# Performance work log

Measured on AMD Instinct MI355X. Metric: run time of the kernel, lower is better.

## Reference

```python
import jax, jax.numpy as jnp
import numpy as np

N_NODES = 100000


def _sage_conv(x, edge_index, w_l, w_r, b):
    # PyG SAGEConv (mean aggr, root_weight=True):
    #   out_i = W_l @ mean_{j in N(i)} x_j + b + W_r @ x_i
    # edge_index[0] = source nodes, edge_index[1] = destination nodes.
    src, dst = edge_index[0], edge_index[1]
    msgs = x[src]  # [E, C_in]
    summed = jax.ops.segment_sum(msgs, dst, num_segments=N_NODES)  # [N, C_in]
    deg = jax.ops.segment_sum(jnp.ones((src.shape[0],), x.dtype), dst,
                              num_segments=N_NODES)
    mean = summed / jnp.maximum(deg, 1.0)[:, None]
    return mean @ w_l.T + b + x @ w_r.T


def setup_inputs() -> dict:
    key = jax.random.key(0)
    ks = jax.random.split(key, 12)
    C_IN, C_H, C_OUT = 32, 64, 1
    E = 1600000

    def glorot(k, shape):
        fan_in = shape[1]
        return jax.random.uniform(k, shape, jnp.float32,
                                  -1.0 / np.sqrt(fan_in), 1.0 / np.sqrt(fan_in))

    x = jax.random.normal(ks[0], (N_NODES, C_IN), jnp.float32)
    edge_index = jax.random.randint(ks[1], (2, E), 0, N_NODES, jnp.int64)
    return {
        "x": x,
        "edge_index": edge_index,
        "w_l1": glorot(ks[2], (C_H, C_IN)),
        "w_r1": glorot(ks[3], (C_H, C_IN)),
        "b1": jnp.zeros((C_H,), jnp.float32),
        "w_l2": glorot(ks[4], (C_H, C_H)),
        "w_r2": glorot(ks[5], (C_H, C_H)),
        "b2": jnp.zeros((C_H,), jnp.float32),
        "w_l3": glorot(ks[6], (C_OUT, C_H)),
        "w_r3": glorot(ks[7], (C_OUT, C_H)),
        "b3": jnp.zeros((C_OUT,), jnp.float32),
    }


def reference(x, edge_index, w_l1, w_r1, b1, w_l2, w_r2, b2, w_l3, w_r3, b3):
    h = jax.nn.relu(_sage_conv(x, edge_index, w_l1, w_r1, b1))
    h = jax.nn.relu(_sage_conv(h, edge_index, w_l2, w_r2, b2))
    h = _sage_conv(h, edge_index, w_l3, w_r3, b3)
    return jax.nn.sigmoid(h)
```

## Files before the change

kernel.cpp:

```cpp
#include <hip/hip_runtime.h>
#include <math.h>

#define NN 100000
#define CAP 48
#define ZROW NN
#define XCONV_NB 3125

#define PART_NB 1024
#define STRIDE4 (PART_NB * 256 * 4)
#define BUKN 256
#define NBUK 391
#define NREP 8
#define LCAPR 768

typedef float  v4f __attribute__((ext_vector_type(4)));
typedef int    v4i __attribute__((ext_vector_type(4)));
typedef float  v2f __attribute__((ext_vector_type(2)));

__device__ __forceinline__ unsigned short f2bf(float v) {
    unsigned int u = __float_as_uint(v);
    u += 0x7FFFu + ((u >> 16) & 1u);
    return (unsigned short)(u >> 16);
}
__device__ __forceinline__ float bf2f(unsigned short b) {
    return __uint_as_float(((unsigned int)b) << 16);
}
__device__ __forceinline__ float bflo(unsigned int u) {
    return __uint_as_float(u << 16);
}
__device__ __forceinline__ float bfhi(unsigned int u) {
    return __uint_as_float(u & 0xFFFF0000u);
}
__device__ __forceinline__ unsigned int pack2bf(float a, float b) {
    return (unsigned)f2bf(a) | ((unsigned)f2bf(b) << 16);
}

__global__ __launch_bounds__(256) void part_kernel(
    const int* __restrict__ ei, int* __restrict__ gcur, unsigned int* __restrict__ lists,
    int E, const float* __restrict__ x, unsigned char* __restrict__ xf8,
    unsigned char* __restrict__ h1f8, int xtotal) {
    if (blockIdx.x >= PART_NB) {
        int t = threadIdx.x;
        if (blockIdx.x == PART_NB) {
            if (t < 16) ((unsigned int*)(h1f8 + (size_t)NN * 64))[t] = 0;
            else if (t < 24) ((unsigned int*)(xf8 + (size_t)NN * 32))[t - 16] = 0;
        }
        int i = ((blockIdx.x - PART_NB) * 256 + t) * 4;
        if (i + 3 < xtotal) {
            float4 v = *(const float4*)(x + i);
            int w = __builtin_amdgcn_cvt_pk_fp8_f32(v.x, v.y, 0, false);
            w = __builtin_amdgcn_cvt_pk_fp8_f32(v.z, v.w, w, true);
            *(unsigned int*)(xf8 + i) = (unsigned int)w;
        } else if (i < xtotal) {
            for (int j = i; j < xtotal; ++j) {
                int w = __builtin_amdgcn_cvt_pk_fp8_f32(x[j], 0.f, 0, false);
                xf8[j] = (unsigned char)(w & 0xFF);
            }
        }
        return;
    }
    __shared__ int lcnt[NBUK], lbase[NBUK];
    int t = threadIdx.x;
    for (int i = t; i < NBUK; i += 256) lcnt[i] = 0;
    __syncthreads();

    const int* dsts = ei + E;
    unsigned int ent[8];
    int eb[8], rk[8];
    bool val[8];
    int base0 = (blockIdx.x * 256 + t) * 4;
    int rep = blockIdx.x & (NREP - 1);

#pragma unroll
    for (int it = 0; it < 2; ++it) {
        int e0 = base0 + it * STRIDE4;
        if (e0 + 3 < E) {
            v4i d = *(const v4i*)(dsts + e0);
            v4i s = *(const v4i*)(ei + e0);
            int dd[4] = {d.x, d.y, d.z, d.w};
            int ss[4] = {s.x, s.y, s.z, s.w};
#pragma unroll
            for (int j = 0; j < 4; ++j) {
                int k = it * 4 + j;
                int b = dd[j] >> 8;
                eb[k] = b;
                ent[k] = ((unsigned int)(dd[j] & 255) << 17) | (unsigned int)ss[j];
                val[k] = true;
                rk[k] = atomicAdd(&lcnt[b], 1);
            }
        } else {
#pragma unroll
            for (int j = 0; j < 4; ++j) {
                int k = it * 4 + j;
                int e = e0 + j;
                val[k] = (e < E);
                eb[k] = 0; ent[k] = 0; rk[k] = 0;
                if (e < E) {
                    int dv = dsts[e];
                    int b = dv >> 8;
                    eb[k] = b;
                    ent[k] = ((unsigned int)(dv & 255) << 17) | (unsigned int)ei[e];
                    rk[k] = atomicAdd(&lcnt[b], 1);
                }
            }
        }
    }
    __syncthreads();
    for (int i = t; i < NBUK; i += 256)
        lbase[i] = atomicAdd(&gcur[rep * NBUK + i], lcnt[i]);
    __syncthreads();
#pragma unroll
    for (int k = 0; k < 8; ++k) {
        if (val[k]) {
            int pos = lbase[eb[k]] + rk[k];
            if (pos < LCAPR)
                lists[((size_t)eb[k] * NREP + rep) * LCAPR + pos] = ent[k];
        }
    }
}

__global__ __launch_bounds__(256) void fill_kernel(
    const unsigned int* __restrict__ lists, const int* __restrict__ gcur,
    int* __restrict__ cnt, int* __restrict__ csr) {
    __shared__ int lc[BUKN];
    __shared__ int tile[BUKN * CAP];
    int b = blockIdx.x, t = threadIdx.x;
    lc[t] = 0;
    for (int i = t; i < BUKN * CAP; i += 256) tile[i] = ZROW;
    __syncthreads();
    for (int rep = 0; rep < NREP; ++rep) {
        int total = gcur[rep * NBUK + b];
        if (total > LCAPR) total = LCAPR;
        const unsigned int* lg = lists + ((size_t)b * NREP + rep) * LCAPR;
        for (int e = t; e < total; e += 256) {
            unsigned int ent = lg[e];
            int dl = (int)(ent >> 17);
            int pos = atomicAdd(&lc[dl], 1);
            if (pos < CAP) tile[dl * CAP + pos] = (int)(ent & 0x1FFFFu);
        }
    }
    __syncthreads();
    int nodes = NN - b * BUKN;
    if (nodes > BUKN) nodes = BUKN;
    if (t < nodes) cnt[b * BUKN + t] = lc[t];
    int tot = nodes * CAP;
    int gbase = b * BUKN * CAP;
    for (int i = t * 4; i < tot; i += 1024)
        *(v4i*)(csr + gbase + i) = *(const v4i*)(tile + i);
}


__global__ __launch_bounds__(256) void agg1_kernel(
    const unsigned char* __restrict__ xf8, const int* __restrict__ cnt,
    const int* __restrict__ csr, unsigned int* __restrict__ mean1b, int n) {
    int t = threadIdx.x;
    int lane = t & 63, wv = t >> 6;
    int p = lane & 7, q = lane >> 3;
    int ngrp = (n + 3) >> 2;
    for (int grp = blockIdx.x; grp < ngrp; grp += gridDim.x) {
        int node = __builtin_amdgcn_readfirstlane(grp * 4 + wv);
        if (node >= n) continue;
        int deg = cnt[node];
        int len = (deg < CAP) ? deg : CAP;
        int lenp = (len + 31) & ~31;
        int base = node * CAP;
        float aA[4] = {0.f, 0.f, 0.f, 0.f}, aB[4] = {0.f, 0.f, 0.f, 0.f};
        float aC[4] = {0.f, 0.f, 0.f, 0.f}, aD[4] = {0.f, 0.f, 0.f, 0.f};
        for (int i = 0; i < lenp; i += 32) {
            int i0 = __builtin_nontemporal_load(csr + base + i + q);
            int i1 = __builtin_nontemporal_load(csr + base + i + 8 + q);
            int i2 = __builtin_nontemporal_load(csr + base + i + 16 + q);
            int i3 = __builtin_nontemporal_load(csr + base + i + 24 + q);
            unsigned int u0 = *(const unsigned int*)(xf8 + (size_t)i0 * 32 + 4 * p);
            unsigned int u1 = *(const unsigned int*)(xf8 + (size_t)i1 * 32 + 4 * p);
            unsigned int u2 = *(const unsigned int*)(xf8 + (size_t)i2 * 32 + 4 * p);
            unsigned int u3 = *(const unsigned int*)(xf8 + (size_t)i3 * 32 + 4 * p);
            v2f l0 = __builtin_amdgcn_cvt_pk_f32_fp8((int)u0, false);
            v2f h0 = __builtin_amdgcn_cvt_pk_f32_fp8((int)u0, true);
            v2f l1 = __builtin_amdgcn_cvt_pk_f32_fp8((int)u1, false);
            v2f h1 = __builtin_amdgcn_cvt_pk_f32_fp8((int)u1, true);
            v2f l2 = __builtin_amdgcn_cvt_pk_f32_fp8((int)u2, false);
            v2f h2 = __builtin_amdgcn_cvt_pk_f32_fp8((int)u2, true);
            v2f l3 = __builtin_amdgcn_cvt_pk_f32_fp8((int)u3, false);
            v2f h3 = __builtin_amdgcn_cvt_pk_f32_fp8((int)u3, true);
            aA[0] += l0.x; aA[1] += l0.y; aA[2] += h0.x; aA[3] += h0.y;
            aB[0] += l1.x; aB[1] += l1.y; aB[2] += h1.x; aB[3] += h1.y;
            aC[0] += l2.x; aC[1] += l2.y; aC[2] += h2.x; aC[3] += h2.y;
            aD[0] += l3.x; aD[1] += l3.y; aD[2] += h3.x; aD[3] += h3.y;
        }
        float s[4];
#pragma unroll
        for (int k = 0; k < 4; ++k) {
            float v = (aA[k] + aB[k]) + (aC[k] + aD[k]);
            v += __shfl_xor(v, 8, 64);
            v += __shfl_xor(v, 16, 64);
            v += __shfl_xor(v, 32, 64);
            s[k] = v;
        }
        float inv = 1.0f / (float)(deg > 1 ? deg : 1);
        if (q == 0) {
            uint2 o;
            o.x = pack2bf(s[0] * inv, s[1] * inv);
            o.y = pack2bf(s[2] * inv, s[3] * inv);
            *(uint2*)(mean1b + (size_t)node * 16 + p * 2) = o;
        }
    }
}

__global__ __launch_bounds__(256) void agg2_kernel(
    const unsigned char* __restrict__ h1f8, const int* __restrict__ cnt,
    const int* __restrict__ csr, unsigned int* __restrict__ mean2b, int n) {
    int t = threadIdx.x;
    int lane = t & 63, wv = t >> 6;
    int p = lane & 15, q = lane >> 4;
    int ngrp = (n + 3) >> 2;
    for (int grp = blockIdx.x; grp < ngrp; grp += gridDim.x) {
        int node = __builtin_amdgcn_readfirstlane(grp * 4 + wv);
        if (node >= n) continue;
        int deg = cnt[node];
        int len = (deg < CAP) ? deg : CAP;
        int lenp = (len + 15) & ~15;
        int base = node * CAP;
        float aA[4] = {0.f, 0.f, 0.f, 0.f}, aB[4] = {0.f, 0.f, 0.f, 0.f};
        float aC[4] = {0.f, 0.f, 0.f, 0.f}, aD[4] = {0.f, 0.f, 0.f, 0.f};
        for (int i = 0; i < lenp; i += 16) {
            int i0 = __builtin_nontemporal_load(csr + base + i + q);
            int i1 = __builtin_nontemporal_load(csr + base + i + 4 + q);
            int i2 = __builtin_nontemporal_load(csr + base + i + 8 + q);
            int i3 = __builtin_nontemporal_load(csr + base + i + 12 + q);
            unsigned int u0 = *(const unsigned int*)(h1f8 + (size_t)i0 * 64 + 4 * p);
            unsigned int u1 = *(const unsigned int*)(h1f8 + (size_t)i1 * 64 + 4 * p);
            unsigned int u2 = *(const unsigned int*)(h1f8 + (size_t)i2 * 64 + 4 * p);
            unsigned int u3 = *(const unsigned int*)(h1f8 + (size_t)i3 * 64 + 4 * p);
            v2f l0 = __builtin_amdgcn_cvt_pk_f32_fp8((int)u0, false);
            v2f h0 = __builtin_amdgcn_cvt_pk_f32_fp8((int)u0, true);
            v2f l1 = __builtin_amdgcn_cvt_pk_f32_fp8((int)u1, false);
            v2f h1 = __builtin_amdgcn_cvt_pk_f32_fp8((int)u1, true);
            v2f l2 = __builtin_amdgcn_cvt_pk_f32_fp8((int)u2, false);
            v2f h2 = __builtin_amdgcn_cvt_pk_f32_fp8((int)u2, true);
            v2f l3 = __builtin_amdgcn_cvt_pk_f32_fp8((int)u3, false);
            v2f h3 = __builtin_amdgcn_cvt_pk_f32_fp8((int)u3, true);
            aA[0] += l0.x; aA[1] += l0.y; aA[2] += h0.x; aA[3] += h0.y;
            aB[0] += l1.x; aB[1] += l1.y; aB[2] += h1.x; aB[3] += h1.y;
            aC[0] += l2.x; aC[1] += l2.y; aC[2] += h2.x; aC[3] += h2.y;
            aD[0] += l3.x; aD[1] += l3.y; aD[2] += h3.x; aD[3] += h3.y;
        }
        float s[4];
#pragma unroll
        for (int k = 0; k < 4; ++k) {
            float v = (aA[k] + aB[k]) + (aC[k] + aD[k]);
            v += __shfl_xor(v, 16, 64);
            v += __shfl_xor(v, 32, 64);
            s[k] = v;
        }
        float inv = 1.0f / (float)(deg > 1 ? deg : 1);
        if (q == 0) {
            uint2 o;
            o.x = pack2bf(s[0] * inv, s[1] * inv);
            o.y = pack2bf(s[2] * inv, s[3] * inv);
            *(uint2*)(mean2b + (size_t)node * 32 + p * 2) = o;
        }
    }
}

template<int HALF, bool FINAL, bool A1BF>
__global__ __launch_bounds__(256) void lin_kernel(
    const unsigned short* __restrict__ a0b,
    const float* __restrict__ a1f, const unsigned short* __restrict__ a1b,
    const float* __restrict__ w0, const float* __restrict__ w1,
    const float* __restrict__ bias,
    const float* __restrict__ wl3, const float* __restrict__ wr3,
    unsigned short* __restrict__ outb, unsigned char* __restrict__ outf8,
    float* __restrict__ z, float* __restrict__ r, int n) {
    const int KC = 32;
    const int K = 2 * HALF;
    __shared__ float A_s[KC * 132];
    __shared__ float B_s[KC * 68];
    int t = threadIdx.x;
    int tx = t & 7;
    int ty = t >> 3;
    int oc0 = tx * 8;
    int node0 = ty * 4;
    int nb = blockIdx.x * 128;
    float acc[4][8];
#pragma unroll
    for (int i = 0; i < 4; ++i)
#pragma unroll
        for (int j = 0; j < 8; ++j) acc[i][j] = 0.f;

    for (int c = 0; c < K / KC; ++c) {
        int koff = c * KC;
        bool useA1 = (koff >= HALF);
        const float* wsrc = useA1 ? w1 : w0;
        int klo = koff % HALF;
        __syncthreads();
        for (int i = t * 4; i < 128 * KC; i += 1024) {
            int nd = i >> 5, kk = i & 31;
            int gnode = nb + nd;
            float v0 = 0.f, v1 = 0.f, v2 = 0.f, v3 = 0.f;
            if (gnode < n) {
                if (!useA1) {
                    uint2 u = *(const uint2*)(a0b + (size_t)gnode * HALF + klo + kk);
                    v0 = bflo(u.x); v1 = bfhi(u.x); v2 = bflo(u.y); v3 = bfhi(u.y);
                } else if (A1BF) {
                    uint2 u = *(const uint2*)(a1b + (size_t)gnode * HALF + klo + kk);
                    v0 = bflo(u.x); v1 = bfhi(u.x); v2 = bflo(u.y); v3 = bfhi(u.y);
                } else {
                    float4 f = *(const float4*)(a1f + (size_t)gnode * HALF + klo + kk);
                    v0 = f.x; v1 = f.y; v2 = f.z; v3 = f.w;
                }
            }
            A_s[kk * 132 + nd] = v0;
            A_s[(kk + 1) * 132 + nd] = v1;
            A_s[(kk + 2) * 132 + nd] = v2;
            A_s[(kk + 3) * 132 + nd] = v3;
        }
        for (int i = t * 4; i < 64 * KC; i += 1024) {
            int oc = i >> 5, kk = i & 31;
            float4 f = *(const float4*)(wsrc + oc * HALF + klo + kk);
            B_s[kk * 68 + oc] = f.x;
            B_s[(kk + 1) * 68 + oc] = f.y;
            B_s[(kk + 2) * 68 + oc] = f.z;
            B_s[(kk + 3) * 68 + oc] = f.w;
        }
        __syncthreads();
#pragma unroll 8
        for (int kk = 0; kk < KC; ++kk) {
            float4 av = *(const float4*)&A_s[kk * 132 + node0];
            float4 b0 = *(const float4*)&B_s[kk * 68 + oc0];
            float4 b1v = *(const float4*)&B_s[kk * 68 + oc0 + 4];
            float aa[4] = {av.x, av.y, av.z, av.w};
            float bb[8] = {b0.x, b0.y, b0.z, b0.w, b1v.x, b1v.y, b1v.z, b1v.w};
#pragma unroll
            for (int i = 0; i < 4; ++i)
#pragma unroll
                for (int j = 0; j < 8; ++j) acc[i][j] += aa[i] * bb[j];
        }
    }

    float bv[8];
#pragma unroll
    for (int j = 0; j < 8; ++j) bv[j] = bias[oc0 + j];

    if (!FINAL) {
#pragma unroll
        for (int i = 0; i < 4; ++i) {
            int node = nb + node0 + i;
            if (node < n) {
                float o[8];
#pragma unroll
                for (int j = 0; j < 8; ++j) o[j] = fmaxf(acc[i][j] + bv[j], 0.f);
                uint4 pk;
                pk.x = pack2bf(o[0], o[1]);
                pk.y = pack2bf(o[2], o[3]);
                pk.z = pack2bf(o[4], o[5]);
                pk.w = pack2bf(o[6], o[7]);
                *(uint4*)&outb[(size_t)node * 64 + oc0] = pk;
                int w0i = __builtin_amdgcn_cvt_pk_fp8_f32(o[0], o[1], 0, false);
                w0i = __builtin_amdgcn_cvt_pk_fp8_f32(o[2], o[3], w0i, true);
                int w1i = __builtin_amdgcn_cvt_pk_fp8_f32(o[4], o[5], 0, false);
                w1i = __builtin_amdgcn_cvt_pk_fp8_f32(o[6], o[7], w1i, true);
                uint2 pk8;
                pk8.x = (unsigned int)w0i;
                pk8.y = (unsigned int)w1i;
                *(uint2*)(outf8 + (size_t)node * 64 + oc0) = pk8;
            }
        }
    } else {
        float w3l[8], w3r[8];
#pragma unroll
        for (int j = 0; j < 8; ++j) { w3l[j] = wl3[oc0 + j]; w3r[j] = wr3[oc0 + j]; }
#pragma unroll
        for (int i = 0; i < 4; ++i) {
            float zz = 0.f, rr = 0.f;
#pragma unroll
            for (int j = 0; j < 8; ++j) {
                float h2 = fmaxf(acc[i][j] + bv[j], 0.f);
                zz += h2 * w3l[j];
                rr += h2 * w3r[j];
            }
#pragma unroll
            for (int o = 1; o < 8; o <<= 1) {
                zz += __shfl_xor(zz, o, 64);
                rr += __shfl_xor(rr, o, 64);
            }
            int node = nb + node0 + i;
            if (tx == 0 && node < n) { z[node] = zz; r[node] = rr; }
        }
    }
}

__global__ void final_kernel(const float* __restrict__ z, const float* __restrict__ r,
                             const int* __restrict__ cnt, const int* __restrict__ csr,
                             const float* __restrict__ b3, float* __restrict__ out, int n) {
    int t = threadIdx.x;
    int lane = t & 63, wv = t >> 6;
    int node = __builtin_amdgcn_readfirstlane(blockIdx.x * 4 + wv);
    if (node >= n) return;
    int deg = cnt[node];
    int len = (deg < CAP) ? deg : CAP;
    float acc = 0.f;
    if (lane < len) acc = z[csr[node * CAP + lane]];
#pragma unroll
    for (int o = 32; o > 0; o >>= 1) acc += __shfl_down(acc, o, 64);
    if (lane == 0) {
        float m = acc / (float)(deg > 1 ? deg : 1);
        out[node] = 1.0f / (1.0f + expf(-(m + r[node] + b3[0])));
    }
}

extern "C" void kernel_launch(void* const* d_in, const int* in_sizes, int n_in,
                              void* d_out, int out_size, void* d_ws, size_t ws_size,
                              hipStream_t stream) {
    const float* x   = (const float*)d_in[0];
    const int*   ei  = (const int*)d_in[1];
    const float* wl1 = (const float*)d_in[2];
    const float* wr1 = (const float*)d_in[3];
    const float* b1  = (const float*)d_in[4];
    const float* wl2 = (const float*)d_in[5];
    const float* wr2 = (const float*)d_in[6];
    const float* b2  = (const float*)d_in[7];
    const float* wl3 = (const float*)d_in[8];
    const float* wr3 = (const float*)d_in[9];
    const float* b3  = (const float*)d_in[10];
    float* out = (float*)d_out;

    const int E = in_sizes[1] / 2;
    const int n = NN;

    int* cnt = (int*)d_ws;
    int* gcur = cnt + n;
    int* csr = gcur + NREP * NBUK + 8;
    float* z = (float*)(csr + (size_t)n * CAP);
    float* r = z + n;
    unsigned char*  xf8 = (unsigned char*)(r + n);
    unsigned short* h1b = (unsigned short*)(xf8 + (size_t)(n + 1) * 32);
    unsigned char*  h1f8 = (unsigned char*)(h1b + (size_t)(n + 1) * 64);
    unsigned short* mb  = (unsigned short*)(h1f8 + (size_t)(n + 1) * 64);
    unsigned int* lists = (unsigned int*)mb;

    hipMemsetAsync(gcur, 0, sizeof(int) * (NREP * NBUK + 8), stream);
    part_kernel<<<PART_NB + XCONV_NB, 256, 0, stream>>>(ei, gcur, lists, E, x, xf8, h1f8, n * 32);
    fill_kernel<<<NBUK, 256, 0, stream>>>(lists, gcur, cnt, csr);

    int gemm_grid = (n + 127) / 128;

    agg1_kernel<<<2048, 256, 0, stream>>>(xf8, cnt, csr, (unsigned int*)mb, n);
    lin_kernel<32, false, false><<<gemm_grid, 256, 0, stream>>>(
        mb, x, nullptr, wl1, wr1, b1, nullptr, nullptr, h1b, h1f8, nullptr, nullptr, n);

    agg2_kernel<<<2048, 256, 0, stream>>>(h1f8, cnt, csr, (unsigned int*)mb, n);
    lin_kernel<64, true, true><<<gemm_grid, 256, 0, stream>>>(
        mb, nullptr, h1b, wl2, wr2, b2, wl3, wr3, nullptr, nullptr, z, r, n);

    final_kernel<<<(n + 3) / 4, 256, 0, stream>>>(z, r, cnt, csr, b3, out, n);
}
```

Measured before the change: 251.9 us.

## Fuse neighbor mean aggregation into the linear GEMM kernels via shared memory

Merges the separate aggregation kernels into the SAGE linear kernels. Each 128-node block now computes its own neighbor means from the fp8 features and stores them as bf16 in shared memory instead of writing them to global memory and reading them back. This removes a global round trip of the mean tensor and two kernel launches. The cost is extra shared memory and a long serial aggregation phase per block before the GEMM, which may lower occupancy and latency hiding compared with the 2048-block grid-stride aggregation.

```diff
diff --git a/kernel.cpp b/kernel.cpp
--- a/kernel.cpp
+++ b/kernel.cpp
@@ -149,124 +149,11 @@
         *(v4i*)(csr + gbase + i) = *(const v4i*)(tile + i);
 }
 
-
-__global__ __launch_bounds__(256) void agg1_kernel(
-    const unsigned char* __restrict__ xf8, const int* __restrict__ cnt,
-    const int* __restrict__ csr, unsigned int* __restrict__ mean1b, int n) {
-    int t = threadIdx.x;
-    int lane = t & 63, wv = t >> 6;
-    int p = lane & 7, q = lane >> 3;
-    int ngrp = (n + 3) >> 2;
-    for (int grp = blockIdx.x; grp < ngrp; grp += gridDim.x) {
-        int node = __builtin_amdgcn_readfirstlane(grp * 4 + wv);
-        if (node >= n) continue;
-        int deg = cnt[node];
-        int len = (deg < CAP) ? deg : CAP;
-        int lenp = (len + 31) & ~31;
-        int base = node * CAP;
-        float aA[4] = {0.f, 0.f, 0.f, 0.f}, aB[4] = {0.f, 0.f, 0.f, 0.f};
-        float aC[4] = {0.f, 0.f, 0.f, 0.f}, aD[4] = {0.f, 0.f, 0.f, 0.f};
-        for (int i = 0; i < lenp; i += 32) {
-            int i0 = __builtin_nontemporal_load(csr + base + i + q);
-            int i1 = __builtin_nontemporal_load(csr + base + i + 8 + q);
-            int i2 = __builtin_nontemporal_load(csr + base + i + 16 + q);
-            int i3 = __builtin_nontemporal_load(csr + base + i + 24 + q);
-            unsigned int u0 = *(const unsigned int*)(xf8 + (size_t)i0 * 32 + 4 * p);
-            unsigned int u1 = *(const unsigned int*)(xf8 + (size_t)i1 * 32 + 4 * p);
-            unsigned int u2 = *(const unsigned int*)(xf8 + (size_t)i2 * 32 + 4 * p);
-            unsigned int u3 = *(const unsigned int*)(xf8 + (size_t)i3 * 32 + 4 * p);
-            v2f l0 = __builtin_amdgcn_cvt_pk_f32_fp8((int)u0, false);
-            v2f h0 = __builtin_amdgcn_cvt_pk_f32_fp8((int)u0, true);
-            v2f l1 = __builtin_amdgcn_cvt_pk_f32_fp8((int)u1, false);
-            v2f h1 = __builtin_amdgcn_cvt_pk_f32_fp8((int)u1, true);
-            v2f l2 = __builtin_amdgcn_cvt_pk_f32_fp8((int)u2, false);
-            v2f h2 = __builtin_amdgcn_cvt_pk_f32_fp8((int)u2, true);
-            v2f l3 = __builtin_amdgcn_cvt_pk_f32_fp8((int)u3, false);
-            v2f h3 = __builtin_amdgcn_cvt_pk_f32_fp8((int)u3, true);
-            aA[0] += l0.x; aA[1] += l0.y; aA[2] += h0.x; aA[3] += h0.y;
-            aB[0] += l1.x; aB[1] += l1.y; aB[2] += h1.x; aB[3] += h1.y;
-            aC[0] += l2.x; aC[1] += l2.y; aC[2] += h2.x; aC[3] += h2.y;
-            aD[0] += l3.x; aD[1] += l3.y; aD[2] += h3.x; aD[3] += h3.y;
-        }
-        float s[4];
-#pragma unroll
-        for (int k = 0; k < 4; ++k) {
-            float v = (aA[k] + aB[k]) + (aC[k] + aD[k]);
-            v += __shfl_xor(v, 8, 64);
-            v += __shfl_xor(v, 16, 64);
-            v += __shfl_xor(v, 32, 64);
-            s[k] = v;
-        }
-        float inv = 1.0f / (float)(deg > 1 ? deg : 1);
-        if (q == 0) {
-            uint2 o;
-            o.x = pack2bf(s[0] * inv, s[1] * inv);
-            o.y = pack2bf(s[2] * inv, s[3] * inv);
-            *(uint2*)(mean1b + (size_t)node * 16 + p * 2) = o;
-        }
-    }
-}
-
-__global__ __launch_bounds__(256) void agg2_kernel(
-    const unsigned char* __restrict__ h1f8, const int* __restrict__ cnt,
-    const int* __restrict__ csr, unsigned int* __restrict__ mean2b, int n) {
-    int t = threadIdx.x;
-    int lane = t & 63, wv = t >> 6;
-    int p = lane & 15, q = lane >> 4;
-    int ngrp = (n + 3) >> 2;
-    for (int grp = blockIdx.x; grp < ngrp; grp += gridDim.x) {
-        int node = __builtin_amdgcn_readfirstlane(grp * 4 + wv);
-        if (node >= n) continue;
-        int deg = cnt[node];
-        int len = (deg < CAP) ? deg : CAP;
-        int lenp = (len + 15) & ~15;
-        int base = node * CAP;
-        float aA[4] = {0.f, 0.f, 0.f, 0.f}, aB[4] = {0.f, 0.f, 0.f, 0.f};
-        float aC[4] = {0.f, 0.f, 0.f, 0.f}, aD[4] = {0.f, 0.f, 0.f, 0.f};
-        for (int i = 0; i < lenp; i += 16) {
-            int i0 = __builtin_nontemporal_load(csr + base + i + q);
-            int i1 = __builtin_nontemporal_load(csr + base + i + 4 + q);
-            int i2 = __builtin_nontemporal_load(csr + base + i + 8 + q);
-            int i3 = __builtin_nontemporal_load(csr + base + i + 12 + q);
-            unsigned int u0 = *(const unsigned int*)(h1f8 + (size_t)i0 * 64 + 4 * p);
-            unsigned int u1 = *(const unsigned int*)(h1f8 + (size_t)i1 * 64 + 4 * p);
-            unsigned int u2 = *(const unsigned int*)(h1f8 + (size_t)i2 * 64 + 4 * p);
-            unsigned int u3 = *(const unsigned int*)(h1f8 + (size_t)i3 * 64 + 4 * p);
-            v2f l0 = __builtin_amdgcn_cvt_pk_f32_fp8((int)u0, false);
-            v2f h0 = __builtin_amdgcn_cvt_pk_f32_fp8((int)u0, true);
-            v2f l1 = __builtin_amdgcn_cvt_pk_f32_fp8((int)u1, false);
-            v2f h1 = __builtin_amdgcn_cvt_pk_f32_fp8((int)u1, true);
-            v2f l2 = __builtin_amdgcn_cvt_pk_f32_fp8((int)u2, false);
-            v2f h2 = __builtin_amdgcn_cvt_pk_f32_fp8((int)u2, true);
-            v2f l3 = __builtin_amdgcn_cvt_pk_f32_fp8((int)u3, false);
-            v2f h3 = __builtin_amdgcn_cvt_pk_f32_fp8((int)u3, true);
-            aA[0] += l0.x; aA[1] += l0.y; aA[2] += h0.x; aA[3] += h0.y;
-            aB[0] += l1.x; aB[1] += l1.y; aB[2] += h1.x; aB[3] += h1.y;
-            aC[0] += l2.x; aC[1] += l2.y; aC[2] += h2.x; aC[3] += h2.y;
-            aD[0] += l3.x; aD[1] += l3.y; aD[2] += h3.x; aD[3] += h3.y;
-        }
-        float s[4];
-#pragma unroll
-        for (int k = 0; k < 4; ++k) {
-            float v = (aA[k] + aB[k]) + (aC[k] + aD[k]);
-            v += __shfl_xor(v, 16, 64);
-            v += __shfl_xor(v, 32, 64);
-            s[k] = v;
-        }
-        float inv = 1.0f / (float)(deg > 1 ? deg : 1);
-        if (q == 0) {
-            uint2 o;
-            o.x = pack2bf(s[0] * inv, s[1] * inv);
-            o.y = pack2bf(s[2] * inv, s[3] * inv);
-            *(uint2*)(mean2b + (size_t)node * 32 + p * 2) = o;
-        }
-    }
-}
-
-template<int HALF, bool FINAL, bool A1BF>
-__global__ __launch_bounds__(256) void lin_kernel(
-    const unsigned short* __restrict__ a0b,
-    const float* __restrict__ a1f, const unsigned short* __restrict__ a1b,
+template<int HALF, bool FINAL>
+__global__ __launch_bounds__(256) void flin_kernel(
+    const unsigned char* __restrict__ gf8,
+    const float* __restrict__ selff, const unsigned short* __restrict__ selfb,
+    const int* __restrict__ cnt, const int* __restrict__ csr,
     const float* __restrict__ w0, const float* __restrict__ w1,
     const float* __restrict__ bias,
     const float* __restrict__ wl3, const float* __restrict__ wr3,
@@ -274,14 +161,115 @@
     float* __restrict__ z, float* __restrict__ r, int n) {
     const int KC = 32;
     const int K = 2 * HALF;
+    __shared__ unsigned int M_su[(HALF / 2) * 132];
     __shared__ float A_s[KC * 132];
     __shared__ float B_s[KC * 68];
     int t = threadIdx.x;
+    int lane = t & 63, wv = t >> 6;
+    int nb = blockIdx.x * 128;
+
+    if (HALF == 32) {
+        int p = lane & 7, q = lane >> 3;
+        for (int g = 0; g < 32; ++g) {
+            int rnd = g * 4 + wv;
+            int node = nb + rnd;
+            int deg = (node < n) ? cnt[node] : 0;
+            int len = (deg < CAP) ? deg : CAP;
+            int lenp = (len + 31) & ~31;
+            int base = node * CAP;
+            float aA[4] = {0.f, 0.f, 0.f, 0.f}, aB[4] = {0.f, 0.f, 0.f, 0.f};
+            float aC[4] = {0.f, 0.f, 0.f, 0.f}, aD[4] = {0.f, 0.f, 0.f, 0.f};
+            for (int i = 0; i < lenp; i += 32) {
+                int i0 = __builtin_nontemporal_load(csr + base + i + q);
+                int i1 = __builtin_nontemporal_load(csr + base + i + 8 + q);
+                int i2 = __builtin_nontemporal_load(csr + base + i + 16 + q);
+                int i3 = __builtin_nontemporal_load(csr + base + i + 24 + q);
+                unsigned int u0 = *(const unsigned int*)(gf8 + (size_t)i0 * 32 + 4 * p);
+                unsigned int u1 = *(const unsigned int*)(gf8 + (size_t)i1 * 32 + 4 * p);
+                unsigned int u2 = *(const unsigned int*)(gf8 + (size_t)i2 * 32 + 4 * p);
+                unsigned int u3 = *(const unsigned int*)(gf8 + (size_t)i3 * 32 + 4 * p);
+                v2f l0 = __builtin_amdgcn_cvt_pk_f32_fp8((int)u0, false);
+                v2f h0 = __builtin_amdgcn_cvt_pk_f32_fp8((int)u0, true);
+                v2f l1 = __builtin_amdgcn_cvt_pk_f32_fp8((int)u1, false);
+                v2f h1 = __builtin_amdgcn_cvt_pk_f32_fp8((int)u1, true);
+                v2f l2 = __builtin_amdgcn_cvt_pk_f32_fp8((int)u2, false);
+                v2f h2 = __builtin_amdgcn_cvt_pk_f32_fp8((int)u2, true);
+                v2f l3 = __builtin_amdgcn_cvt_pk_f32_fp8((int)u3, false);
+                v2f h3 = __builtin_amdgcn_cvt_pk_f32_fp8((int)u3, true);
+                aA[0] += l0.x; aA[1] += l0.y; aA[2] += h0.x; aA[3] += h0.y;
+                aB[0] += l1.x; aB[1] += l1.y; aB[2] += h1.x; aB[3] += h1.y;
+                aC[0] += l2.x; aC[1] += l2.y; aC[2] += h2.x; aC[3] += h2.y;
+                aD[0] += l3.x; aD[1] += l3.y; aD[2] += h3.x; aD[3] += h3.y;
+            }
+            float s[4];
+#pragma unroll
+            for (int k = 0; k < 4; ++k) {
+                float v = (aA[k] + aB[k]) + (aC[k] + aD[k]);
+                v += __shfl_xor(v, 8, 64);
+                v += __shfl_xor(v, 16, 64);
+                v += __shfl_xor(v, 32, 64);
+                s[k] = v;
+            }
+            float inv = 1.0f / (float)(deg > 1 ? deg : 1);
+            if (q == 0) {
+                M_su[(2 * p) * 132 + rnd] = pack2bf(s[0] * inv, s[1] * inv);
+                M_su[(2 * p + 1) * 132 + rnd] = pack2bf(s[2] * inv, s[3] * inv);
+            }
+        }
+    } else {
+        int p = lane & 15, q = lane >> 4;
+        for (int g = 0; g < 32; ++g) {
+            int rnd = g * 4 + wv;
+            int node = nb + rnd;
+            int deg = (node < n) ? cnt[node] : 0;
+            int len = (deg < CAP) ? deg : CAP;
+            int lenp = (len + 15) & ~15;
+            int base = node * CAP;
+            float aA[4] = {0.f, 0.f, 0.f, 0.f}, aB[4] = {0.f, 0.f, 0.f, 0.f};
+            float aC[4] = {0.f, 0.f, 0.f, 0.f}, aD[4] = {0.f, 0.f, 0.f, 0.f};
+            for (int i = 0; i < lenp; i += 16) {
+                int i0 = __builtin_nontemporal_load(csr + base + i + q);
+                int i1 = __builtin_nontemporal_load(csr + base + i + 4 + q);
+                int i2 = __builtin_nontemporal_load(csr + base + i + 8 + q);
+                int i3 = __builtin_nontemporal_load(csr + base + i + 12 + q);
+                unsigned int u0 = *(const unsigned int*)(gf8 + (size_t)i0 * 64 + 4 * p);
+                unsigned int u1 = *(const unsigned int*)(gf8 + (size_t)i1 * 64 + 4 * p);
+                unsigned int u2 = *(const unsigned int*)(gf8 + (size_t)i2 * 64 + 4 * p);
+                unsigned int u3 = *(const unsigned int*)(gf8 + (size_t)i3 * 64 + 4 * p);
+                v2f l0 = __builtin_amdgcn_cvt_pk_f32_fp8((int)u0, false);
+                v2f h0 = __builtin_amdgcn_cvt_pk_f32_fp8((int)u0, true);
+                v2f l1 = __builtin_amdgcn_cvt_pk_f32_fp8((int)u1, false);
+                v2f h1 = __builtin_amdgcn_cvt_pk_f32_fp8((int)u1, true);
+                v2f l2 = __builtin_amdgcn_cvt_pk_f32_fp8((int)u2, false);
+                v2f h2 = __builtin_amdgcn_cvt_pk_f32_fp8((int)u2, true);
+                v2f l3 = __builtin_amdgcn_cvt_pk_f32_fp8((int)u3, false);
+                v2f h3 = __builtin_amdgcn_cvt_pk_f32_fp8((int)u3, true);
+                aA[0] += l0.x; aA[1] += l0.y; aA[2] += h0.x; aA[3] += h0.y;
+                aB[0] += l1.x; aB[1] += l1.y; aB[2] += h1.x; aB[3] += h1.y;
+                aC[0] += l2.x; aC[1] += l2.y; aC[2] += h2.x; aC[3] += h2.y;
+                aD[0] += l3.x; aD[1] += l3.y; aD[2] += h3.x; aD[3] += h3.y;
+            }
+            float s[4];
+#pragma unroll
+            for (int k = 0; k < 4; ++k) {
+                float v = (aA[k] + aB[k]) + (aC[k] + aD[k]);
+                v += __shfl_xor(v, 16, 64);
+                v += __shfl_xor(v, 32, 64);
+                s[k] = v;
+            }
+            float inv = 1.0f / (float)(deg > 1 ? deg : 1);
+            if (q == 0) {
+                M_su[(2 * p) * 132 + rnd] = pack2bf(s[0] * inv, s[1] * inv);
+                M_su[(2 * p + 1) * 132 + rnd] = pack2bf(s[2] * inv, s[3] * inv);
+            }
+        }
+    }
+    __syncthreads();
+
     int tx = t & 7;
     int ty = t >> 3;
     int oc0 = tx * 8;
     int node0 = ty * 4;
-    int nb = blockIdx.x * 128;
     float acc[4][8];
 #pragma unroll
     for (int i = 0; i < 4; ++i)
@@ -290,30 +278,36 @@
 
     for (int c = 0; c < K / KC; ++c) {
         int koff = c * KC;
-        bool useA1 = (koff >= HALF);
-        const float* wsrc = useA1 ? w1 : w0;
+        bool useSelf = (koff >= HALF);
+        const float* wsrc = useSelf ? w1 : w0;
         int klo = koff % HALF;
         __syncthreads();
-        for (int i = t * 4; i < 128 * KC; i += 1024) {
-            int nd = i >> 5, kk = i & 31;
-            int gnode = nb + nd;
-            float v0 = 0.f, v1 = 0.f, v2 = 0.f, v3 = 0.f;
-            if (gnode < n) {
-                if (!useA1) {
-                    uint2 u = *(const uint2*)(a0b + (size_t)gnode * HALF + klo + kk);
-                    v0 = bflo(u.x); v1 = bfhi(u.x); v2 = bflo(u.y); v3 = bfhi(u.y);
-                } else if (A1BF) {
-                    uint2 u = *(const uint2*)(a1b + (size_t)gnode * HALF + klo + kk);
-                    v0 = bflo(u.x); v1 = bfhi(u.x); v2 = bflo(u.y); v3 = bfhi(u.y);
-                } else {
-                    float4 f = *(const float4*)(a1f + (size_t)gnode * HALF + klo + kk);
-                    v0 = f.x; v1 = f.y; v2 = f.z; v3 = f.w;
+        if (!useSelf) {
+            for (int i = t; i < 128 * KC; i += 256) {
+                int nd = i >> 5, kk = i & 31;
+                int kabs = klo + kk;
+                unsigned int u = M_su[(kabs >> 1) * 132 + nd];
+                A_s[kk * 132 + nd] = (kabs & 1) ? bfhi(u) : bflo(u);
+            }
+        } else {
+            for (int i = t * 4; i < 128 * KC; i += 1024) {
+                int nd = i >> 5, kk = i & 31;
+                int gnode = nb + nd;
+                float v0 = 0.f, v1 = 0.f, v2 = 0.f, v3 = 0.f;
+                if (gnode < n) {
+                    if (HALF == 32) {
+                        float4 f = *(const float4*)(selff + (size_t)gnode * HALF + klo + kk);
+                        v0 = f.x; v1 = f.y; v2 = f.z; v3 = f.w;
+                    } else {
+                        uint2 u = *(const uint2*)(selfb + (size_t)gnode * HALF + klo + kk);
+                        v0 = bflo(u.x); v1 = bfhi(u.x); v2 = bflo(u.y); v3 = bfhi(u.y);
+                    }
                 }
-            }
-            A_s[kk * 132 + nd] = v0;
-            A_s[(kk + 1) * 132 + nd] = v1;
-            A_s[(kk + 2) * 132 + nd] = v2;
-            A_s[(kk + 3) * 132 + nd] = v3;
+                A_s[kk * 132 + nd] = v0;
+                A_s[(kk + 1) * 132 + nd] = v1;
+                A_s[(kk + 2) * 132 + nd] = v2;
+                A_s[(kk + 3) * 132 + nd] = v3;
+            }
         }
         for (int i = t * 4; i < 64 * KC; i += 1024) {
             int oc = i >> 5, kk = i & 31;
@@ -436,8 +430,7 @@
     unsigned char*  xf8 = (unsigned char*)(r + n);
     unsigned short* h1b = (unsigned short*)(xf8 + (size_t)(n + 1) * 32);
     unsigned char*  h1f8 = (unsigned char*)(h1b + (size_t)(n + 1) * 64);
-    unsigned short* mb  = (unsigned short*)(h1f8 + (size_t)(n + 1) * 64);
-    unsigned int* lists = (unsigned int*)mb;
+    unsigned int* lists = (unsigned int*)(h1f8 + (size_t)(n + 1) * 64);
 
     hipMemsetAsync(gcur, 0, sizeof(int) * (NREP * NBUK + 8), stream);
     part_kernel<<<PART_NB + XCONV_NB, 256, 0, stream>>>(ei, gcur, lists, E, x, xf8, h1f8, n * 32);
@@ -445,13 +438,13 @@
 
     int gemm_grid = (n + 127) / 128;
 
-    agg1_kernel<<<2048, 256, 0, stream>>>(xf8, cnt, csr, (unsigned int*)mb, n);
-    lin_kernel<32, false, false><<<gemm_grid, 256, 0, stream>>>(
-        mb, x, nullptr, wl1, wr1, b1, nullptr, nullptr, h1b, h1f8, nullptr, nullptr, n);
-
-    agg2_kernel<<<2048, 256, 0, stream>>>(h1f8, cnt, csr, (unsigned int*)mb, n);
-    lin_kernel<64, true, true><<<gemm_grid, 256, 0, stream>>>(
-        mb, nullptr, h1b, wl2, wr2, b2, wl3, wr3, nullptr, nullptr, z, r, n);
+    flin_kernel<32, false><<<gemm_grid, 256, 0, stream>>>(
+        xf8, x, nullptr, cnt, csr, wl1, wr1, b1, nullptr, nullptr,
+        h1b, h1f8, nullptr, nullptr, n);
+
+    flin_kernel<64, true><<<gemm_grid, 256, 0, stream>>>(
+        h1f8, nullptr, h1b, cnt, csr, wl2, wr2, b2, wl3, wr3,
+        nullptr, nullptr, z, r, n);
 
     final_kernel<<<(n + 3) / 4, 256, 0, stream>>>(z, r, cnt, csr, b3, out, n);
 }
```

Result: slower. 339.8 us (+34.9%).
